# Kernel optimization log

Hardware: AMD Instinct MI355X
Metric: run time of the kernel (lower is better)

## Reference

```python
import jax, jax.numpy as jnp
import numpy as np

B, S, F, H = 2, 2048, 1024, 16
HD = F // H


def setup_inputs() -> dict:
    key = jax.random.key(0)
    ks = jax.random.split(key, 9)
    Q = jax.random.normal(ks[0], (B, S, F), dtype=jnp.float32)
    K = jax.random.normal(ks[1], (B, S, F), dtype=jnp.float32)
    V = jax.random.normal(ks[2], (B, S, F), dtype=jnp.float32)
    # additive pre-softmax causal mask: 0 on/below diagonal, -1e9 above
    causal = jnp.tril(jnp.ones((S, S), dtype=bool))
    mask_1 = jnp.where(causal, 0.0, -1e9).astype(jnp.float32)[None, None]
    # multiplicative post-softmax mask in [0,1)
    mask_2 = jax.random.uniform(ks[3], (1, 1, S, S), dtype=jnp.float32)
    scale = 1.0 / np.sqrt(F)
    W_q = jax.random.normal(ks[4], (F, F), dtype=jnp.float32) * scale
    W_k = jax.random.normal(ks[5], (F, F), dtype=jnp.float32) * scale
    W_v = jax.random.normal(ks[6], (F, F), dtype=jnp.float32) * scale
    W_o = jax.random.normal(ks[7], (F, F), dtype=jnp.float32) * scale
    return {"Q": Q, "K": K, "V": V, "mask_1": mask_1, "mask_2": mask_2,
            "W_q": W_q, "W_k": W_k, "W_v": W_v, "W_o": W_o}


def reference(Q, K, V, mask_1, mask_2, W_q, W_k, W_v, W_o):
    # Linear projections (no bias), split into heads: [B,S,F] -> [B,H,S,HD]
    def proj(x, W):
        return (x @ W.T).reshape(B, S, H, HD).transpose(0, 2, 1, 3)
    q, k, v = proj(Q, W_q), proj(K, W_k), proj(V, W_v)
    # scores [B,H,S,S], scaled by sqrt(head_size)
    scores = jnp.einsum('bhqd,bhkd->bhqk', q, k) / np.sqrt(HD)
    scores = scores + mask_1  # additive pre-softmax mask
    probs = jax.nn.softmax(scores, axis=-1) * mask_2  # multiplicative post-softmax mask
    out = jnp.einsum('bhqk,bhkd->bhqd', probs, v)
    out = out.transpose(0, 2, 1, 3).reshape(B, S, F)
    return out @ W_o.T
```

## Files before the change

### kernel.cpp

```cpp
#include <hip/hip_runtime.h>
#include <hip/hip_bf16.h>
#include <stdint.h>

typedef __bf16 bf16_t;
typedef __bf16 bf16x8 __attribute__((ext_vector_type(8)));
typedef __bf16 bf16x4v __attribute__((ext_vector_type(4)));
typedef float f32x4 __attribute__((ext_vector_type(4)));

#define GLDS16(g, l)                                                         \
  __builtin_amdgcn_global_load_lds(                                          \
      (const __attribute__((address_space(1))) void*)(g),                    \
      (__attribute__((address_space(3))) void*)(l), 16, 0, 0)

__device__ __forceinline__ f32x4 mfma16(bf16x8 a, bf16x8 b, f32x4 c) {
  return __builtin_amdgcn_mfma_f32_16x16x32_bf16(a, b, c, 0, 0, 0);
}

static constexpr int S = 2048, F = 1024, H = 16, HD = 64;

static constexpr size_t OFF_QB  = 0;
static constexpr size_t OFF_KB  = 4194304;
static constexpr size_t OFF_VB  = 8388608;
static constexpr size_t OFF_WQ  = 12582912;
static constexpr size_t OFF_WK  = 13631488;
static constexpr size_t OFF_WV  = 14680064;
static constexpr size_t OFF_WO  = 15728640;
static constexpr size_t OFF_QP  = 16777216;
static constexpr size_t OFF_KP  = 20971520;
static constexpr size_t OFF_VPT = 25165824;

__global__ void cvt_all(const float* __restrict__ s0, const float* __restrict__ s1,
                        const float* __restrict__ s2,
                        const float* __restrict__ w0, const float* __restrict__ w1,
                        const float* __restrict__ w2, const float* __restrict__ w3,
                        bf16_t* __restrict__ d0, bf16_t* __restrict__ d1,
                        bf16_t* __restrict__ d2,
                        bf16_t* __restrict__ e0, bf16_t* __restrict__ e1,
                        bf16_t* __restrict__ e2, bf16_t* __restrict__ e3) {
  const float* s;
  bf16_t* d;
  size_t r;
  if (blockIdx.x < 6144) {
    int t = blockIdx.x * 256 + threadIdx.x;
    int a = t >> 19;
    r = (size_t)(t & 0x7FFFF) * 8;
    s = (a == 0) ? s0 : (a == 1) ? s1 : s2;
    d = (a == 0) ? d0 : (a == 1) ? d1 : d2;
  } else {
    int t = (blockIdx.x - 6144) * 256 + threadIdx.x;
    int a = t >> 17;
    r = (size_t)(t & 0x1FFFF) * 8;
    s = (a == 0) ? w0 : (a == 1) ? w1 : (a == 2) ? w2 : w3;
    d = (a == 0) ? e0 : (a == 1) ? e1 : (a == 2) ? e2 : e3;
  }
  const float4* sp = (const float4*)(s + r);
  float4 u = sp[0], v = sp[1];
  bf16x8 o;
  o[0] = (bf16_t)u.x; o[1] = (bf16_t)u.y; o[2] = (bf16_t)u.z; o[3] = (bf16_t)u.w;
  o[4] = (bf16_t)v.x; o[5] = (bf16_t)v.y; o[6] = (bf16_t)v.z; o[7] = (bf16_t)v.w;
  *(bf16x8*)(d + r) = o;
}

__device__ __forceinline__ void stage128x32(const bf16_t* __restrict__ g, int ld,
                                            bf16_t* lds, int wv, int ln) {
#pragma unroll
  for (int i = 0; i < 2; ++i) {
    int ch  = wv * 2 + i;
    int row = ch * 16 + (ln >> 2);
    int col = (ln & 3) * 8;
    GLDS16(g + (size_t)row * ld + col, lds + ch * 512);
  }
}

__global__ __launch_bounds__(256, 2) void proj_gemm(
    const bf16_t* __restrict__ Qb, const bf16_t* __restrict__ Kb, const bf16_t* __restrict__ Vb,
    const bf16_t* __restrict__ Wq, const bf16_t* __restrict__ Wk, const bf16_t* __restrict__ Wv,
    bf16_t* __restrict__ qp, bf16_t* __restrict__ kp, bf16_t* __restrict__ vpT) {
  __shared__ bf16_t As[2][128 * 32];
  __shared__ bf16_t Bs[2][128 * 32];
  const int z = blockIdx.z;
  const bf16_t* A = (z == 0) ? Qb : (z == 1) ? Kb : Vb;
  const bf16_t* W = (z == 0) ? Wq : (z == 1) ? Wk : Wv;
  const int m0 = blockIdx.x * 128, n0 = blockIdx.y * 128;
  const int tid = threadIdx.x, wv = tid >> 6, ln = tid & 63;
  const int wr = wv >> 1, wc = wv & 1, lr = ln & 15, lg = ln >> 4;
  f32x4 acc[4][4];
#pragma unroll
  for (int i = 0; i < 4; ++i)
#pragma unroll
    for (int j = 0; j < 4; ++j) acc[i][j] = (f32x4){0.f, 0.f, 0.f, 0.f};

  stage128x32(A + (size_t)m0 * F, F, As[0], wv, ln);
  stage128x32(W + (size_t)n0 * F, F, Bs[0], wv, ln);
  __syncthreads();

  for (int k0 = 0; k0 < F; k0 += 32) {
    const int cur = (k0 >> 5) & 1;
    if (k0 + 32 < F) {
      stage128x32(A + (size_t)m0 * F + k0 + 32, F, As[cur ^ 1], wv, ln);
      stage128x32(W + (size_t)n0 * F + k0 + 32, F, Bs[cur ^ 1], wv, ln);
    }
    bf16x8 af[4], bfr[4];
#pragma unroll
    for (int i = 0; i < 4; ++i)
      af[i] = *(const bf16x8*)&As[cur][(wr * 64 + i * 16 + lr) * 32 + lg * 8];
#pragma unroll
    for (int j = 0; j < 4; ++j)
      bfr[j] = *(const bf16x8*)&Bs[cur][(wc * 64 + j * 16 + lr) * 32 + lg * 8];
#pragma unroll
    for (int i = 0; i < 4; ++i)
#pragma unroll
      for (int j = 0; j < 4; ++j) acc[i][j] = mfma16(af[i], bfr[j], acc[i][j]);
    __syncthreads();
  }

  const int rbase = m0 + wr * 64, cbase = n0 + wc * 64;
  if (z < 2) {
    bf16_t* out = (z == 0) ? qp : kp;
    const float qscl = (z == 0) ? 0.18033688f : 1.0f;
#pragma unroll
    for (int i = 0; i < 4; ++i)
#pragma unroll
      for (int j = 0; j < 4; ++j) {
        int r0 = rbase + i * 16 + lg * 4;
        int c  = cbase + j * 16 + lr;
        int b = r0 >> 11, s = r0 & 2047, h = c >> 6, d = c & 63;
        size_t base = ((size_t)(b * H + h) * S + s) * HD + d;
#pragma unroll
        for (int reg = 0; reg < 4; ++reg)
          out[base + (size_t)reg * HD] = (bf16_t)(acc[i][j][reg] * qscl);
      }
  } else {
#pragma unroll
    for (int i = 0; i < 4; ++i)
#pragma unroll
      for (int j = 0; j < 4; ++j) {
        int r0 = rbase + i * 16 + lg * 4;
        int c  = cbase + j * 16 + lr;
        int b = r0 >> 11, s = r0 & 2047, h = c >> 6, d = c & 63;
        size_t base = ((size_t)(b * H + h) * HD + d) * S + s;
        bf16x4v pv;
#pragma unroll
        for (int reg = 0; reg < 4; ++reg) pv[reg] = (bf16_t)acc[i][j][reg];
        *(bf16x4v*)&vpT[base] = pv;
      }
  }
}

__global__ __launch_bounds__(256, 2) void out_gemm(
    const bf16_t* __restrict__ PA, const bf16_t* __restrict__ PB,
    const float* __restrict__ lA, const float* __restrict__ lB,
    const bf16_t* __restrict__ W, float* __restrict__ out) {
  __shared__ bf16_t As[2][128 * 32];
  __shared__ bf16_t Bs[2][128 * 32];
  const int m0 = blockIdx.x * 128, n0 = blockIdx.y * 128;
  const int tid = threadIdx.x, wv = tid >> 6, ln = tid & 63;
  const int wr = wv >> 1, wc = wv & 1, lr = ln & 15, lg = ln >> 4;
  const int ar = tid >> 1, ac = (tid & 1) * 16;
  const int row = m0 + ar, s = row & 2047, b = row >> 11;
  const bool hiS = (s >= 1024);
  f32x4 acc[4][4];
#pragma unroll
  for (int i = 0; i < 4; ++i)
#pragma unroll
    for (int j = 0; j < 4; ++j) acc[i][j] = (f32x4){0.f, 0.f, 0.f, 0.f};

  {
    size_t pb0 = ((size_t)(b * 16) * S + s) * HD + ac;
    bf16x8 a0 = *(const bf16x8*)&PA[pb0];
    bf16x8 a1 = *(const bf16x8*)&PA[pb0 + 8];
    float lv = lA[(b * 16) * S + s], lw = 0.f;
    float va[16];
#pragma unroll
    for (int e = 0; e < 8; ++e) { va[e] = (float)a0[e]; va[8 + e] = (float)a1[e]; }
    if (hiS) {
      bf16x8 b0 = *(const bf16x8*)&PB[pb0];
      bf16x8 b1 = *(const bf16x8*)&PB[pb0 + 8];
      lw = lB[(b * 16) * S + s];
#pragma unroll
      for (int e = 0; e < 8; ++e) { va[e] += (float)b0[e]; va[8 + e] += (float)b1[e]; }
    }
    stage128x32(W + (size_t)n0 * F, F, Bs[0], wv, ln);
    float inv = 1.0f / (lv + lw);
    bf16x8 w0, w1;
#pragma unroll
    for (int e = 0; e < 8; ++e) {
      w0[e] = (bf16_t)(va[e] * inv);
      w1[e] = (bf16_t)(va[8 + e] * inv);
    }
    *(bf16x8*)&As[0][ar * 32 + ac] = w0;
    *(bf16x8*)&As[0][ar * 32 + ac + 8] = w1;
  }
  __syncthreads();

  for (int k0 = 0; k0 < F; k0 += 32) {
    const int cur = (k0 >> 5) & 1;
    const bool pre = (k0 + 32 < F);
    bf16x8 a0, a1, pb0v, pb1v;
    float lv = 0.f, lw = 0.f;
    if (pre) {
      const int kn = k0 + 32, h = kn >> 6, d0 = (kn & 63) + ac;
      size_t pbase = ((size_t)(b * 16 + h) * S + s) * HD + d0;
      a0 = *(const bf16x8*)&PA[pbase];
      a1 = *(const bf16x8*)&PA[pbase + 8];
      lv = lA[(b * 16 + h) * S + s];
      if (hiS) {
        pb0v = *(const bf16x8*)&PB[pbase];
        pb1v = *(const bf16x8*)&PB[pbase + 8];
        lw = lB[(b * 16 + h) * S + s];
      }
      stage128x32(W + (size_t)n0 * F + kn, F, Bs[cur ^ 1], wv, ln);
    }
    bf16x8 af[4], bfr[4];
#pragma unroll
    for (int i = 0; i < 4; ++i)
      af[i] = *(const bf16x8*)&As[cur][(wr * 64 + i * 16 + lr) * 32 + lg * 8];
#pragma unroll
    for (int j = 0; j < 4; ++j)
      bfr[j] = *(const bf16x8*)&Bs[cur][(wc * 64 + j * 16 + lr) * 32 + lg * 8];
#pragma unroll
    for (int i = 0; i < 4; ++i)
#pragma unroll
      for (int j = 0; j < 4; ++j) acc[i][j] = mfma16(af[i], bfr[j], acc[i][j]);
    if (pre) {
      float va[16];
#pragma unroll
      for (int e = 0; e < 8; ++e) { va[e] = (float)a0[e]; va[8 + e] = (float)a1[e]; }
      if (hiS) {
#pragma unroll
        for (int e = 0; e < 8; ++e) { va[e] += (float)pb0v[e]; va[8 + e] += (float)pb1v[e]; }
      }
      float inv = 1.0f / (lv + lw);
      bf16x8 w0, w1;
#pragma unroll
      for (int e = 0; e < 8; ++e) {
        w0[e] = (bf16_t)(va[e] * inv);
        w1[e] = (bf16_t)(va[8 + e] * inv);
      }
      *(bf16x8*)&As[cur ^ 1][ar * 32 + ac] = w0;
      *(bf16x8*)&As[cur ^ 1][ar * 32 + ac + 8] = w1;
    }
    __syncthreads();
  }
#pragma unroll
  for (int i = 0; i < 4; ++i)
#pragma unroll
    for (int j = 0; j < 4; ++j) {
      int r0 = m0 + wr * 64 + i * 16 + lg * 4;
      int c  = n0 + wc * 64 + j * 16 + lr;
#pragma unroll
      for (int reg = 0; reg < 4; ++reg)
        out[(size_t)(r0 + reg) * F + c] = acc[i][j][reg];
    }
}

__global__ __launch_bounds__(256, 4) void flash(
    const bf16_t* __restrict__ qp, const bf16_t* __restrict__ kp,
    const bf16_t* __restrict__ vpT, const float* __restrict__ m2f,
    bf16_t* __restrict__ PA, bf16_t* __restrict__ PB,
    float* __restrict__ lA, float* __restrict__ lB) {
  __shared__ bf16_t Ks[2][64 * 64];
  __shared__ bf16_t Vs[2][64 * 64];
  __shared__ bf16_t Pl[4][16 * 64];
  const int ur = blockIdx.x >> 5, bh = blockIdx.x & 31;
  const int grp = ur / 3, rem = ur % 3;
  int qt, kvlo, kvhi;
  if (rem == 2) { qt = 15 - grp; kvlo = 0; kvhi = qt; }
  else {
    qt = 31 - grp;
    int half = (qt + 2) >> 1;
    if (rem == 0) { kvlo = 0; kvhi = half - 1; }
    else          { kvlo = half; kvhi = qt; }
  }
  bf16_t* __restrict__ PO = (rem == 1) ? PB : PA;
  float*  __restrict__ LO = (rem == 1) ? lB : lA;

  const int tid = threadIdx.x, wv = tid >> 6, ln = tid & 63;
  const int lr = ln & 15, lg = ln >> 4;
  const bf16_t* qb = qp + (size_t)bh * S * HD;
  const bf16_t* kb = kp + (size_t)bh * S * HD;
  const bf16_t* vb = vpT + (size_t)bh * HD * S;
  const int q0w = qt * 64 + wv * 16;
  const int qg  = q0w + lr;

  bf16x8 bq[2];
#pragma unroll
  for (int h2 = 0; h2 < 2; ++h2)
    bq[h2] = *(const bf16x8*)&qb[(size_t)qg * HD + h2 * 32 + lg * 8];

  float ls = 0.f;
  f32x4 accv[4];
#pragma unroll
  for (int n = 0; n < 4; ++n) accv[n] = (f32x4){0.f, 0.f, 0.f, 0.f};

  const int srow0 = ln >> 3, scc0 = ln & 7;
  const int pxor = lr & 7;

#pragma unroll
  for (int i = 0; i < 2; ++i) {
    int ch = wv * 2 + i;
    int row = ch * 8 + srow0;
    int scc = scc0 ^ (row & 7);
    GLDS16(kb + (size_t)(kvlo * 64 + row) * HD + scc * 8, Ks[0] + ch * 512);
    GLDS16(vb + (size_t)row * S + kvlo * 64 + scc * 8, Vs[0] + ch * 512);
  }
  __syncthreads();

  for (int kt = kvlo; kt <= kvhi; ++kt) {
    const int k0 = kt * 64;
    const int cur = (kt - kvlo) & 1;

    float4 m2v[4];
#pragma unroll
    for (int c = 0; c < 4; ++c)
      m2v[c] = *(const float4*)&m2f[(size_t)qg * S + k0 + c * 16 + lg * 4];

    if (kt < kvhi) {
      const int kn = k0 + 64;
#pragma unroll
      for (int i = 0; i < 2; ++i) {
        int ch = wv * 2 + i;
        int row = ch * 8 + srow0;
        int scc = scc0 ^ (row & 7);
        GLDS16(kb + (size_t)(kn + row) * HD + scc * 8, Ks[cur ^ 1] + ch * 512);
        GLDS16(vb + (size_t)row * S + kn + scc * 8, Vs[cur ^ 1] + ch * 512);
      }
    }

    f32x4 st[4];
    __builtin_amdgcn_s_setprio(1);
#pragma unroll
    for (int c = 0; c < 4; ++c) {
      int kr = c * 16 + lr;
      int sw = kr & 7;
      bf16x8 ak0 = *(const bf16x8*)&Ks[cur][kr * 64 + ((lg ^ sw) * 8)];
      bf16x8 ak1 = *(const bf16x8*)&Ks[cur][kr * 64 + (((4 + lg) ^ sw) * 8)];
      f32x4 t = (f32x4){0.f, 0.f, 0.f, 0.f};
      t = mfma16(ak0, bq[0], t);
      t = mfma16(ak1, bq[1], t);
      st[c] = t;
    }
    __builtin_amdgcn_s_setprio(0);
    if (kt == qt) {
#pragma unroll
      for (int c = 0; c < 4; ++c)
#pragma unroll
        for (int r = 0; r < 4; ++r) {
          int kgl = k0 + c * 16 + lg * 4 + r;
          if (kgl > qg) st[c][r] = -1e30f;
        }
    }
#pragma unroll
    for (int c = 0; c < 4; ++c) {
      bf16x4v pw;
      float p0 = exp2f(st[c][0]), p1 = exp2f(st[c][1]);
      float p2 = exp2f(st[c][2]), p3 = exp2f(st[c][3]);
      ls += (p0 + p1) + (p2 + p3);
      pw[0] = (bf16_t)(p0 * m2v[c].x);
      pw[1] = (bf16_t)(p1 * m2v[c].y);
      pw[2] = (bf16_t)(p2 * m2v[c].z);
      pw[3] = (bf16_t)(p3 * m2v[c].w);
      int chunk = (2 * c + (lg >> 1)) ^ pxor;
      *(bf16x4v*)&Pl[wv][lr * 64 + chunk * 8 + (lg & 1) * 4] = pw;
    }
    __builtin_amdgcn_s_setprio(1);
#pragma unroll
    for (int kc = 0; kc < 2; ++kc) {
      int pchunk = (4 * kc + lg) ^ pxor;
      bf16x8 pb = *(const bf16x8*)&Pl[wv][lr * 64 + pchunk * 8];
#pragma unroll
      for (int n = 0; n < 4; ++n) {
        int dr = n * 16 + lr;
        int sw = dr & 7;
        bf16x8 av = *(const bf16x8*)&Vs[cur][dr * 64 + (((kc * 4 + lg) ^ sw) * 8)];
        accv[n] = mfma16(av, pb, accv[n]);
      }
    }
    __builtin_amdgcn_s_setprio(0);
    __syncthreads();
  }

  ls += __shfl_xor(ls, 16, 64);
  ls += __shfl_xor(ls, 32, 64);
  if (lg == 0) LO[bh * S + qg] = ls;
#pragma unroll
  for (int n = 0; n < 4; ++n) {
    bf16x4v ov;
#pragma unroll
    for (int r = 0; r < 4; ++r) ov[r] = (bf16_t)accv[n][r];
    *(bf16x4v*)&PO[((size_t)bh * S + qg) * HD + n * 16 + lg * 4] = ov;
  }
}

extern "C" void kernel_launch(void* const* d_in, const int* in_sizes, int n_in,
                              void* d_out, int out_size, void* d_ws, size_t ws_size,
                              hipStream_t stream) {
  (void)in_sizes; (void)n_in; (void)out_size; (void)ws_size;
  const float* Q  = (const float*)d_in[0];
  const float* K  = (const float*)d_in[1];
  const float* V  = (const float*)d_in[2];
  const float* M2 = (const float*)d_in[4];
  const float* Wq = (const float*)d_in[5];
  const float* Wk = (const float*)d_in[6];
  const float* Wv = (const float*)d_in[7];
  const float* Wo = (const float*)d_in[8];
  bf16_t* ws = (bf16_t*)d_ws;

  bf16_t *Qb = ws + OFF_QB, *Kb = ws + OFF_KB, *Vb = ws + OFF_VB;
  bf16_t *WqB = ws + OFF_WQ, *WkB = ws + OFF_WK, *WvB = ws + OFF_WV, *WoB = ws + OFF_WO;
  bf16_t *qpB = ws + OFF_QP, *kpB = ws + OFF_KP, *vpT = ws + OFF_VPT;
  bf16_t *PA = ws + OFF_KB, *PB = ws + OFF_VB;
  float  *lA = (float*)(ws + OFF_WQ), *lB = (float*)(ws + OFF_WK);

  cvt_all<<<8192, 256, 0, stream>>>(Q, K, V, Wq, Wk, Wv, Wo,
                                    Qb, Kb, Vb, WqB, WkB, WvB, WoB);
  proj_gemm<<<dim3(32, 8, 3), 256, 0, stream>>>(Qb, Kb, Vb, WqB, WkB, WvB, qpB, kpB, vpT);
  flash<<<dim3(1536), 256, 0, stream>>>(qpB, kpB, vpT, M2, PA, PB, lA, lB);
  out_gemm<<<dim3(32, 8), 256, 0, stream>>>(PA, PB, lA, lB, WoB, (float*)d_out);
}
```

Baseline: 146.0 us.

## Use 128-row query tiles with table-driven three-way KV split in flash attention

The flash kernel now uses 512-thread blocks covering 128 query rows (8 waves), so each staged K/V tile is shared by twice as many waves. Work units come from a constant table that splits long causal rows into up to three KV ranges, written to PA/PB/PC partial buffers. The out-projection GEMM sums up to three partials per row. This aims to cut K/V reload traffic and balance causal work, at the cost of idle waves on diagonal tiles, more partial-buffer traffic, and a hand-built schedule table.

```diff
diff --git a/kernel.cpp b/kernel.cpp
--- a/kernel.cpp
+++ b/kernel.cpp
@@ -28,6 +28,19 @@
 static constexpr size_t OFF_QP  = 16777216;
 static constexpr size_t OFF_KP  = 20971520;
 static constexpr size_t OFF_VPT = 25165824;
+
+__device__ __constant__ uint32_t UNIT_TBL[30] = {
+  0x0005000Bu, 0x000B000Bu, 0x010B0C17u,
+  0x000F000Au, 0x010F0B15u, 0x000A000Au, 0x010A0B15u,
+  0x020F161Fu, 0x000E0009u, 0x010E0A13u, 0x020E141Du,
+  0x000D0009u, 0x010D0A13u, 0x00090009u, 0x01090A13u,
+  0x00040009u,
+  0x000C0008u, 0x010C0911u, 0x00080008u, 0x01080911u,
+  0x020D141Bu, 0x020C1219u, 0x00070007u, 0x0107080Fu,
+  0x00030007u,
+  0x00060006u, 0x0106070Du,
+  0x00020005u, 0x00010003u, 0x00000001u
+};
 
 __global__ void cvt_all(const float* __restrict__ s0, const float* __restrict__ s1,
                         const float* __restrict__ s2,
@@ -149,7 +162,9 @@
 
 __global__ __launch_bounds__(256, 2) void out_gemm(
     const bf16_t* __restrict__ PA, const bf16_t* __restrict__ PB,
+    const bf16_t* __restrict__ PC,
     const float* __restrict__ lA, const float* __restrict__ lB,
+    const float* __restrict__ lC,
     const bf16_t* __restrict__ W, float* __restrict__ out) {
   __shared__ bf16_t As[2][128 * 32];
   __shared__ bf16_t Bs[2][128 * 32];
@@ -158,7 +173,8 @@
   const int wr = wv >> 1, wc = wv & 1, lr = ln & 15, lg = ln >> 4;
   const int ar = tid >> 1, ac = (tid & 1) * 16;
   const int row = m0 + ar, s = row & 2047, b = row >> 11;
-  const bool hiS = (s >= 1024);
+  const int g = s >> 7;
+  const int ns = (g < 6) ? 1 : (g < 12) ? 2 : 3;
   f32x4 acc[4][4];
 #pragma unroll
   for (int i = 0; i < 4; ++i)
@@ -169,19 +185,26 @@
     size_t pb0 = ((size_t)(b * 16) * S + s) * HD + ac;
     bf16x8 a0 = *(const bf16x8*)&PA[pb0];
     bf16x8 a1 = *(const bf16x8*)&PA[pb0 + 8];
-    float lv = lA[(b * 16) * S + s], lw = 0.f;
+    float l = lA[(b * 16) * S + s];
     float va[16];
 #pragma unroll
     for (int e = 0; e < 8; ++e) { va[e] = (float)a0[e]; va[8 + e] = (float)a1[e]; }
-    if (hiS) {
+    if (ns >= 2) {
       bf16x8 b0 = *(const bf16x8*)&PB[pb0];
       bf16x8 b1 = *(const bf16x8*)&PB[pb0 + 8];
-      lw = lB[(b * 16) * S + s];
+      l += lB[(b * 16) * S + s];
 #pragma unroll
       for (int e = 0; e < 8; ++e) { va[e] += (float)b0[e]; va[8 + e] += (float)b1[e]; }
     }
+    if (ns >= 3) {
+      bf16x8 c0 = *(const bf16x8*)&PC[pb0];
+      bf16x8 c1 = *(const bf16x8*)&PC[pb0 + 8];
+      l += lC[(b * 16) * S + s];
+#pragma unroll
+      for (int e = 0; e < 8; ++e) { va[e] += (float)c0[e]; va[8 + e] += (float)c1[e]; }
+    }
     stage128x32(W + (size_t)n0 * F, F, Bs[0], wv, ln);
-    float inv = 1.0f / (lv + lw);
+    float inv = 1.0f / l;
     bf16x8 w0, w1;
 #pragma unroll
     for (int e = 0; e < 8; ++e) {
@@ -196,18 +219,23 @@
   for (int k0 = 0; k0 < F; k0 += 32) {
     const int cur = (k0 >> 5) & 1;
     const bool pre = (k0 + 32 < F);
-    bf16x8 a0, a1, pb0v, pb1v;
-    float lv = 0.f, lw = 0.f;
+    bf16x8 a0, a1, b0, b1, c0, c1;
+    float l = 0.f;
     if (pre) {
       const int kn = k0 + 32, h = kn >> 6, d0 = (kn & 63) + ac;
       size_t pbase = ((size_t)(b * 16 + h) * S + s) * HD + d0;
       a0 = *(const bf16x8*)&PA[pbase];
       a1 = *(const bf16x8*)&PA[pbase + 8];
-      lv = lA[(b * 16 + h) * S + s];
-      if (hiS) {
-        pb0v = *(const bf16x8*)&PB[pbase];
-        pb1v = *(const bf16x8*)&PB[pbase + 8];
-        lw = lB[(b * 16 + h) * S + s];
+      l = lA[(b * 16 + h) * S + s];
+      if (ns >= 2) {
+        b0 = *(const bf16x8*)&PB[pbase];
+        b1 = *(const bf16x8*)&PB[pbase + 8];
+        l += lB[(b * 16 + h) * S + s];
+      }
+      if (ns >= 3) {
+        c0 = *(const bf16x8*)&PC[pbase];
+        c1 = *(const bf16x8*)&PC[pbase + 8];
+        l += lC[(b * 16 + h) * S + s];
       }
       stage128x32(W + (size_t)n0 * F + kn, F, Bs[cur ^ 1], wv, ln);
     }
@@ -226,11 +254,15 @@
       float va[16];
 #pragma unroll
       for (int e = 0; e < 8; ++e) { va[e] = (float)a0[e]; va[8 + e] = (float)a1[e]; }
-      if (hiS) {
-#pragma unroll
-        for (int e = 0; e < 8; ++e) { va[e] += (float)pb0v[e]; va[8 + e] += (float)pb1v[e]; }
-      }
-      float inv = 1.0f / (lv + lw);
+      if (ns >= 2) {
+#pragma unroll
+        for (int e = 0; e < 8; ++e) { va[e] += (float)b0[e]; va[8 + e] += (float)b1[e]; }
+      }
+      if (ns >= 3) {
+#pragma unroll
+        for (int e = 0; e < 8; ++e) { va[e] += (float)c0[e]; va[8 + e] += (float)c1[e]; }
+      }
+      float inv = 1.0f / l;
       bf16x8 w0, w1;
 #pragma unroll
       for (int e = 0; e < 8; ++e) {
@@ -254,34 +286,29 @@
     }
 }
 
-__global__ __launch_bounds__(256, 4) void flash(
+__global__ __launch_bounds__(512, 6) void flash(
     const bf16_t* __restrict__ qp, const bf16_t* __restrict__ kp,
     const bf16_t* __restrict__ vpT, const float* __restrict__ m2f,
-    bf16_t* __restrict__ PA, bf16_t* __restrict__ PB,
-    float* __restrict__ lA, float* __restrict__ lB) {
+    bf16_t* __restrict__ PA, bf16_t* __restrict__ PB, bf16_t* __restrict__ PC,
+    float* __restrict__ lA, float* __restrict__ lB, float* __restrict__ lC) {
   __shared__ bf16_t Ks[2][64 * 64];
   __shared__ bf16_t Vs[2][64 * 64];
-  __shared__ bf16_t Pl[4][16 * 64];
+  __shared__ bf16_t Pl[8][16 * 64];
   const int ur = blockIdx.x >> 5, bh = blockIdx.x & 31;
-  const int grp = ur / 3, rem = ur % 3;
-  int qt, kvlo, kvhi;
-  if (rem == 2) { qt = 15 - grp; kvlo = 0; kvhi = qt; }
-  else {
-    qt = 31 - grp;
-    int half = (qt + 2) >> 1;
-    if (rem == 0) { kvlo = 0; kvhi = half - 1; }
-    else          { kvlo = half; kvhi = qt; }
-  }
-  bf16_t* __restrict__ PO = (rem == 1) ? PB : PA;
-  float*  __restrict__ LO = (rem == 1) ? lB : lA;
+  const uint32_t e = UNIT_TBL[ur];
+  const int kvhi = e & 0xFF, kvlo = (e >> 8) & 0xFF;
+  const int g = (e >> 16) & 0xFF, part = (int)(e >> 24);
+  bf16_t* __restrict__ PO = (part == 0) ? PA : (part == 1) ? PB : PC;
+  float*  __restrict__ LO = (part == 0) ? lA : (part == 1) ? lB : lC;
 
   const int tid = threadIdx.x, wv = tid >> 6, ln = tid & 63;
   const int lr = ln & 15, lg = ln >> 4;
   const bf16_t* qb = qp + (size_t)bh * S * HD;
   const bf16_t* kb = kp + (size_t)bh * S * HD;
   const bf16_t* vb = vpT + (size_t)bh * HD * S;
-  const int q0w = qt * 64 + wv * 16;
+  const int q0w = g * 128 + wv * 16;
   const int qg  = q0w + lr;
+  const int dt  = q0w >> 6;
 
   bf16x8 bq[2];
 #pragma unroll
@@ -296,87 +323,86 @@
   const int srow0 = ln >> 3, scc0 = ln & 7;
   const int pxor = lr & 7;
 
-#pragma unroll
-  for (int i = 0; i < 2; ++i) {
-    int ch = wv * 2 + i;
-    int row = ch * 8 + srow0;
+  {
+    int row = wv * 8 + srow0;
     int scc = scc0 ^ (row & 7);
-    GLDS16(kb + (size_t)(kvlo * 64 + row) * HD + scc * 8, Ks[0] + ch * 512);
-    GLDS16(vb + (size_t)row * S + kvlo * 64 + scc * 8, Vs[0] + ch * 512);
+    GLDS16(kb + (size_t)(kvlo * 64 + row) * HD + scc * 8, Ks[0] + wv * 512);
+    GLDS16(vb + (size_t)row * S + kvlo * 64 + scc * 8, Vs[0] + wv * 512);
   }
   __syncthreads();
 
   for (int kt = kvlo; kt <= kvhi; ++kt) {
     const int k0 = kt * 64;
     const int cur = (kt - kvlo) & 1;
+    const bool act = (kt <= dt);
 
     float4 m2v[4];
-#pragma unroll
-    for (int c = 0; c < 4; ++c)
-      m2v[c] = *(const float4*)&m2f[(size_t)qg * S + k0 + c * 16 + lg * 4];
+    if (act) {
+#pragma unroll
+      for (int c = 0; c < 4; ++c)
+        m2v[c] = *(const float4*)&m2f[(size_t)qg * S + k0 + c * 16 + lg * 4];
+    }
 
     if (kt < kvhi) {
       const int kn = k0 + 64;
-#pragma unroll
-      for (int i = 0; i < 2; ++i) {
-        int ch = wv * 2 + i;
-        int row = ch * 8 + srow0;
-        int scc = scc0 ^ (row & 7);
-        GLDS16(kb + (size_t)(kn + row) * HD + scc * 8, Ks[cur ^ 1] + ch * 512);
-        GLDS16(vb + (size_t)row * S + kn + scc * 8, Vs[cur ^ 1] + ch * 512);
-      }
-    }
-
-    f32x4 st[4];
-    __builtin_amdgcn_s_setprio(1);
-#pragma unroll
-    for (int c = 0; c < 4; ++c) {
-      int kr = c * 16 + lr;
-      int sw = kr & 7;
-      bf16x8 ak0 = *(const bf16x8*)&Ks[cur][kr * 64 + ((lg ^ sw) * 8)];
-      bf16x8 ak1 = *(const bf16x8*)&Ks[cur][kr * 64 + (((4 + lg) ^ sw) * 8)];
-      f32x4 t = (f32x4){0.f, 0.f, 0.f, 0.f};
-      t = mfma16(ak0, bq[0], t);
-      t = mfma16(ak1, bq[1], t);
-      st[c] = t;
-    }
-    __builtin_amdgcn_s_setprio(0);
-    if (kt == qt) {
-#pragma unroll
-      for (int c = 0; c < 4; ++c)
-#pragma unroll
-        for (int r = 0; r < 4; ++r) {
-          int kgl = k0 + c * 16 + lg * 4 + r;
-          if (kgl > qg) st[c][r] = -1e30f;
+      int row = wv * 8 + srow0;
+      int scc = scc0 ^ (row & 7);
+      GLDS16(kb + (size_t)(kn + row) * HD + scc * 8, Ks[cur ^ 1] + wv * 512);
+      GLDS16(vb + (size_t)row * S + kn + scc * 8, Vs[cur ^ 1] + wv * 512);
+    }
+
+    if (act) {
+      f32x4 st[4];
+      __builtin_amdgcn_s_setprio(1);
+#pragma unroll
+      for (int c = 0; c < 4; ++c) {
+        int kr = c * 16 + lr;
+        int sw = kr & 7;
+        bf16x8 ak0 = *(const bf16x8*)&Ks[cur][kr * 64 + ((lg ^ sw) * 8)];
+        bf16x8 ak1 = *(const bf16x8*)&Ks[cur][kr * 64 + (((4 + lg) ^ sw) * 8)];
+        f32x4 t = (f32x4){0.f, 0.f, 0.f, 0.f};
+        t = mfma16(ak0, bq[0], t);
+        t = mfma16(ak1, bq[1], t);
+        st[c] = t;
+      }
+      __builtin_amdgcn_s_setprio(0);
+      if (kt == dt) {
+#pragma unroll
+        for (int c = 0; c < 4; ++c)
+#pragma unroll
+          for (int r = 0; r < 4; ++r) {
+            int kgl = k0 + c * 16 + lg * 4 + r;
+            if (kgl > qg) st[c][r] = -1e30f;
+          }
+      }
+#pragma unroll
+      for (int c = 0; c < 4; ++c) {
+        bf16x4v pw;
+        float p0 = exp2f(st[c][0]), p1 = exp2f(st[c][1]);
+        float p2 = exp2f(st[c][2]), p3 = exp2f(st[c][3]);
+        ls += (p0 + p1) + (p2 + p3);
+        pw[0] = (bf16_t)(p0 * m2v[c].x);
+        pw[1] = (bf16_t)(p1 * m2v[c].y);
+        pw[2] = (bf16_t)(p2 * m2v[c].z);
+        pw[3] = (bf16_t)(p3 * m2v[c].w);
+        int chunk = (2 * c + (lg >> 1)) ^ pxor;
+        *(bf16x4v*)&Pl[wv][lr * 64 + chunk * 8 + (lg & 1) * 4] = pw;
+      }
+      __builtin_amdgcn_s_setprio(1);
+#pragma unroll
+      for (int kc = 0; kc < 2; ++kc) {
+        int pchunk = (4 * kc + lg) ^ pxor;
+        bf16x8 pb = *(const bf16x8*)&Pl[wv][lr * 64 + pchunk * 8];
+#pragma unroll
+        for (int n = 0; n < 4; ++n) {
+          int dr = n * 16 + lr;
+          int sw = dr & 7;
+          bf16x8 av = *(const bf16x8*)&Vs[cur][dr * 64 + (((kc * 4 + lg) ^ sw) * 8)];
+          accv[n] = mfma16(av, pb, accv[n]);
         }
-    }
-#pragma unroll
-    for (int c = 0; c < 4; ++c) {
-      bf16x4v pw;
-      float p0 = exp2f(st[c][0]), p1 = exp2f(st[c][1]);
-      float p2 = exp2f(st[c][2]), p3 = exp2f(st[c][3]);
-      ls += (p0 + p1) + (p2 + p3);
-      pw[0] = (bf16_t)(p0 * m2v[c].x);
-      pw[1] = (bf16_t)(p1 * m2v[c].y);
-      pw[2] = (bf16_t)(p2 * m2v[c].z);
-      pw[3] = (bf16_t)(p3 * m2v[c].w);
-      int chunk = (2 * c + (lg >> 1)) ^ pxor;
-      *(bf16x4v*)&Pl[wv][lr * 64 + chunk * 8 + (lg & 1) * 4] = pw;
-    }
-    __builtin_amdgcn_s_setprio(1);
-#pragma unroll
-    for (int kc = 0; kc < 2; ++kc) {
-      int pchunk = (4 * kc + lg) ^ pxor;
-      bf16x8 pb = *(const bf16x8*)&Pl[wv][lr * 64 + pchunk * 8];
-#pragma unroll
-      for (int n = 0; n < 4; ++n) {
-        int dr = n * 16 + lr;
-        int sw = dr & 7;
-        bf16x8 av = *(const bf16x8*)&Vs[cur][dr * 64 + (((kc * 4 + lg) ^ sw) * 8)];
-        accv[n] = mfma16(av, pb, accv[n]);
-      }
-    }
-    __builtin_amdgcn_s_setprio(0);
+      }
+      __builtin_amdgcn_s_setprio(0);
+    }
     __syncthreads();
   }
 
@@ -409,12 +435,13 @@
   bf16_t *Qb = ws + OFF_QB, *Kb = ws + OFF_KB, *Vb = ws + OFF_VB;
   bf16_t *WqB = ws + OFF_WQ, *WkB = ws + OFF_WK, *WvB = ws + OFF_WV, *WoB = ws + OFF_WO;
   bf16_t *qpB = ws + OFF_QP, *kpB = ws + OFF_KP, *vpT = ws + OFF_VPT;
-  bf16_t *PA = ws + OFF_KB, *PB = ws + OFF_VB;
+  bf16_t *PA = ws + OFF_KB, *PB = ws + OFF_VB, *PC = ws + OFF_QB;
   float  *lA = (float*)(ws + OFF_WQ), *lB = (float*)(ws + OFF_WK);
+  float  *lC = (float*)(ws + OFF_WV);
 
   cvt_all<<<8192, 256, 0, stream>>>(Q, K, V, Wq, Wk, Wv, Wo,
                                     Qb, Kb, Vb, WqB, WkB, WvB, WoB);
   proj_gemm<<<dim3(32, 8, 3), 256, 0, stream>>>(Qb, Kb, Vb, WqB, WkB, WvB, qpB, kpB, vpT);
-  flash<<<dim3(1536), 256, 0, stream>>>(qpB, kpB, vpT, M2, PA, PB, lA, lB);
-  out_gemm<<<dim3(32, 8), 256, 0, stream>>>(PA, PB, lA, lB, WoB, (float*)d_out);
-}
+  flash<<<dim3(960), 512, 0, stream>>>(qpB, kpB, vpT, M2, PA, PB, PC, lA, lB, lC);
+  out_gemm<<<dim3(32, 8), 256, 0, stream>>>(PA, PB, PC, lA, lB, lC, WoB, (float*)d_out);
+}
```

New measurement: 179.2 us. 22.8% more time.

## Fuse fp32-to-bf16 activation conversion into projection GEMM staging

Applied to the files above, without the earlier changes.

The projection GEMM now loads fp32 Q/K/V tiles directly into LDS with an XOR-swizzled layout and converts them to bf16 in registers before the MFMA. The separate activation conversion pass is dropped, so only the weights are still pre-converted. This removes a full read/write round trip of the activations. In exchange, LDS use for the A tile doubles and the inner loop gains conversion ALU work, while launch bounds are raised to 3 blocks per SM for both GEMMs.

```diff
diff --git a/kernel.cpp b/kernel.cpp
--- a/kernel.cpp
+++ b/kernel.cpp
@@ -18,9 +18,8 @@
 
 static constexpr int S = 2048, F = 1024, H = 16, HD = 64;
 
-static constexpr size_t OFF_QB  = 0;
-static constexpr size_t OFF_KB  = 4194304;
-static constexpr size_t OFF_VB  = 8388608;
+static constexpr size_t OFF_PA  = 4194304;
+static constexpr size_t OFF_PB  = 8388608;
 static constexpr size_t OFF_WQ  = 12582912;
 static constexpr size_t OFF_WK  = 13631488;
 static constexpr size_t OFF_WV  = 14680064;
@@ -29,30 +28,15 @@
 static constexpr size_t OFF_KP  = 20971520;
 static constexpr size_t OFF_VPT = 25165824;
 
-__global__ void cvt_all(const float* __restrict__ s0, const float* __restrict__ s1,
-                        const float* __restrict__ s2,
-                        const float* __restrict__ w0, const float* __restrict__ w1,
-                        const float* __restrict__ w2, const float* __restrict__ w3,
-                        bf16_t* __restrict__ d0, bf16_t* __restrict__ d1,
-                        bf16_t* __restrict__ d2,
-                        bf16_t* __restrict__ e0, bf16_t* __restrict__ e1,
-                        bf16_t* __restrict__ e2, bf16_t* __restrict__ e3) {
-  const float* s;
-  bf16_t* d;
-  size_t r;
-  if (blockIdx.x < 6144) {
-    int t = blockIdx.x * 256 + threadIdx.x;
-    int a = t >> 19;
-    r = (size_t)(t & 0x7FFFF) * 8;
-    s = (a == 0) ? s0 : (a == 1) ? s1 : s2;
-    d = (a == 0) ? d0 : (a == 1) ? d1 : d2;
-  } else {
-    int t = (blockIdx.x - 6144) * 256 + threadIdx.x;
-    int a = t >> 17;
-    r = (size_t)(t & 0x1FFFF) * 8;
-    s = (a == 0) ? w0 : (a == 1) ? w1 : (a == 2) ? w2 : w3;
-    d = (a == 0) ? e0 : (a == 1) ? e1 : (a == 2) ? e2 : e3;
-  }
+__global__ void cvt_w4(const float* __restrict__ w0, const float* __restrict__ w1,
+                       const float* __restrict__ w2, const float* __restrict__ w3,
+                       bf16_t* __restrict__ e0, bf16_t* __restrict__ e1,
+                       bf16_t* __restrict__ e2, bf16_t* __restrict__ e3) {
+  int t = blockIdx.x * 256 + threadIdx.x;
+  int a = t >> 17;
+  size_t r = (size_t)(t & 0x1FFFF) * 8;
+  const float* s = (a == 0) ? w0 : (a == 1) ? w1 : (a == 2) ? w2 : w3;
+  bf16_t* d = (a == 0) ? e0 : (a == 1) ? e1 : (a == 2) ? e2 : e3;
   const float4* sp = (const float4*)(s + r);
   float4 u = sp[0], v = sp[1];
   bf16x8 o;
@@ -72,14 +56,25 @@
   }
 }
 
-__global__ __launch_bounds__(256, 2) void proj_gemm(
-    const bf16_t* __restrict__ Qb, const bf16_t* __restrict__ Kb, const bf16_t* __restrict__ Vb,
+__device__ __forceinline__ void stageA128x32_f32(const float* __restrict__ g, int ld,
+                                                 float* lds, int wv, int ln) {
+#pragma unroll
+  for (int i = 0; i < 4; ++i) {
+    int ch  = wv * 4 + i;
+    int row = ch * 8 + (ln >> 3);
+    int scc = (ln & 7) ^ (row & 7);
+    GLDS16(g + (size_t)row * ld + scc * 4, lds + ch * 256);
+  }
+}
+
+__global__ __launch_bounds__(256, 3) void proj_gemm(
+    const float* __restrict__ Qf, const float* __restrict__ Kf, const float* __restrict__ Vf,
     const bf16_t* __restrict__ Wq, const bf16_t* __restrict__ Wk, const bf16_t* __restrict__ Wv,
     bf16_t* __restrict__ qp, bf16_t* __restrict__ kp, bf16_t* __restrict__ vpT) {
-  __shared__ bf16_t As[2][128 * 32];
+  __shared__ float  Af[2][128 * 32];
   __shared__ bf16_t Bs[2][128 * 32];
   const int z = blockIdx.z;
-  const bf16_t* A = (z == 0) ? Qb : (z == 1) ? Kb : Vb;
+  const float* A = (z == 0) ? Qf : (z == 1) ? Kf : Vf;
   const bf16_t* W = (z == 0) ? Wq : (z == 1) ? Wk : Wv;
   const int m0 = blockIdx.x * 128, n0 = blockIdx.y * 128;
   const int tid = threadIdx.x, wv = tid >> 6, ln = tid & 63;
@@ -90,20 +85,29 @@
 #pragma unroll
     for (int j = 0; j < 4; ++j) acc[i][j] = (f32x4){0.f, 0.f, 0.f, 0.f};
 
-  stage128x32(A + (size_t)m0 * F, F, As[0], wv, ln);
+  stageA128x32_f32(A + (size_t)m0 * F, F, Af[0], wv, ln);
   stage128x32(W + (size_t)n0 * F, F, Bs[0], wv, ln);
   __syncthreads();
 
   for (int k0 = 0; k0 < F; k0 += 32) {
     const int cur = (k0 >> 5) & 1;
     if (k0 + 32 < F) {
-      stage128x32(A + (size_t)m0 * F + k0 + 32, F, As[cur ^ 1], wv, ln);
+      stageA128x32_f32(A + (size_t)m0 * F + k0 + 32, F, Af[cur ^ 1], wv, ln);
       stage128x32(W + (size_t)n0 * F + k0 + 32, F, Bs[cur ^ 1], wv, ln);
     }
     bf16x8 af[4], bfr[4];
 #pragma unroll
-    for (int i = 0; i < 4; ++i)
-      af[i] = *(const bf16x8*)&As[cur][(wr * 64 + i * 16 + lr) * 32 + lg * 8];
+    for (int i = 0; i < 4; ++i) {
+      int r = wr * 64 + i * 16 + lr;
+      int sx = r & 7;
+      f32x4 lo = *(const f32x4*)&Af[cur][r * 32 + (((lg * 2)     ^ sx) * 4)];
+      f32x4 hi = *(const f32x4*)&Af[cur][r * 32 + (((lg * 2 + 1) ^ sx) * 4)];
+#pragma unroll
+      for (int e = 0; e < 4; ++e) {
+        af[i][e]     = (bf16_t)lo[e];
+        af[i][4 + e] = (bf16_t)hi[e];
+      }
+    }
 #pragma unroll
     for (int j = 0; j < 4; ++j)
       bfr[j] = *(const bf16x8*)&Bs[cur][(wc * 64 + j * 16 + lr) * 32 + lg * 8];
@@ -147,7 +151,7 @@
   }
 }
 
-__global__ __launch_bounds__(256, 2) void out_gemm(
+__global__ __launch_bounds__(256, 3) void out_gemm(
     const bf16_t* __restrict__ PA, const bf16_t* __restrict__ PB,
     const float* __restrict__ lA, const float* __restrict__ lB,
     const bf16_t* __restrict__ W, float* __restrict__ out) {
@@ -406,15 +410,13 @@
   const float* Wo = (const float*)d_in[8];
   bf16_t* ws = (bf16_t*)d_ws;
 
-  bf16_t *Qb = ws + OFF_QB, *Kb = ws + OFF_KB, *Vb = ws + OFF_VB;
   bf16_t *WqB = ws + OFF_WQ, *WkB = ws + OFF_WK, *WvB = ws + OFF_WV, *WoB = ws + OFF_WO;
   bf16_t *qpB = ws + OFF_QP, *kpB = ws + OFF_KP, *vpT = ws + OFF_VPT;
-  bf16_t *PA = ws + OFF_KB, *PB = ws + OFF_VB;
+  bf16_t *PA = ws + OFF_PA, *PB = ws + OFF_PB;
   float  *lA = (float*)(ws + OFF_WQ), *lB = (float*)(ws + OFF_WK);
 
-  cvt_all<<<8192, 256, 0, stream>>>(Q, K, V, Wq, Wk, Wv, Wo,
-                                    Qb, Kb, Vb, WqB, WkB, WvB, WoB);
-  proj_gemm<<<dim3(32, 8, 3), 256, 0, stream>>>(Qb, Kb, Vb, WqB, WkB, WvB, qpB, kpB, vpT);
+  cvt_w4<<<2048, 256, 0, stream>>>(Wq, Wk, Wv, Wo, WqB, WkB, WvB, WoB);
+  proj_gemm<<<dim3(32, 8, 3), 256, 0, stream>>>(Q, K, V, WqB, WkB, WvB, qpB, kpB, vpT);
   flash<<<dim3(1536), 256, 0, stream>>>(qpB, kpB, vpT, M2, PA, PB, lA, lB);
   out_gemm<<<dim3(32, 8), 256, 0, stream>>>(PA, PB, lA, lB, WoB, (float*)d_out);
 }
```

Result: faster. 137.7 us (-5.6%).
